# Optimization experiments

Measured on AMD Instinct MI355X. Metric: run time of the kernel, lower is better.

Reference implementation:

```python
import jax, jax.numpy as jnp
import numpy as np

CLAMP_MIN = -10.0
CLAMP_MAX = 10.0
B = 8
N = 100_000
EDGES = 3_200_000


def setup_inputs() -> dict:
    key = jax.random.key(0)
    ks = jax.random.split(key, 9)
    chem_influence = jax.random.normal(ks[0], (B, N), dtype=jnp.float32)
    E = jax.random.normal(ks[1], (B, N), dtype=jnp.float32)
    O = jax.random.normal(ks[2], (B, N), dtype=jnp.float32)
    src = jax.random.randint(ks[3], (EDGES,), 0, N, dtype=jnp.int64) if jax.config.jax_enable_x64 else jax.random.randint(ks[3], (EDGES,), 0, N).astype(jnp.int32)
    dst = jax.random.randint(ks[4], (EDGES,), 0, N).astype(src.dtype)
    w = jax.random.normal(ks[5], (EDGES,), dtype=jnp.float32)
    o_pre = jax.random.normal(ks[6], (B, N), dtype=jnp.float32)
    # learned per-neuron params (rnd_init=True ranges from the module)
    threshold = jax.random.uniform(ks[7], (N,), minval=-1.0, maxval=2.0, dtype=jnp.float32)
    decay = jax.random.uniform(ks[8], (N,), minval=0.05, maxval=1.0, dtype=jnp.float32)
    return {"chem_influence": chem_influence, "E": E, "O": O, "src": src,
            "dst": dst, "w": w, "o_pre": o_pre, "threshold": threshold, "decay": decay}


def reference(chem_influence, E, O, src, dst, w, o_pre, threshold, decay):
    # Gap-junction path: gather presyn output Oj and postsyn internal state En per edge
    Oj = o_pre[:, src]                    # (B, E)
    En = E[:, dst]                        # (B, E)
    contrib = Oj * w * jnp.sign(Oj - En)  # sign(Oj - En) * w_j * Oj
    # scatter-add edge contributions into the chemical-influence buffer (dup indices accumulate)
    chem = chem_influence.at[:, dst].add(contrib)  # (B, N)
    # Neuron dynamics (eqs 10, 11)
    S = jnp.clip(E + chem, CLAMP_MIN, CLAMP_MAX)
    gt = S > threshold
    mask = (~gt) & (S == E)
    new_o = jax.nn.relu(S - threshold)
    new_e = jnp.where(gt, new_o, jnp.where(mask, E - decay, S))
    # torch module returns (new_o, (new_e, new_o)); flatten the state tuple
    return new_o, new_e
```

## Files before the change

### kernel.cpp

```cpp
#include <hip/hip_runtime.h>

#define CLAMP_MIN_F (-10.0f)
#define CLAMP_MAX_F (10.0f)
#define BATCH 8
#define SUP_LOG 8
#define SNODES 256
#define MAXS 512
#define ESTR 9
#define EPB 16384
#define CH 2048
#define TB_BIN 1024
#define TB_ACC 1024
#define RECPT (CH / TB_ACC)
#define SPLIT 2
#define MAX4K 4096

__global__ void prep_o_kernel(const float* __restrict__ o_pre,
                              float* __restrict__ o_preT,
                              unsigned* __restrict__ total,
                              int N) {
    int n = blockIdx.x * blockDim.x + threadIdx.x;
    if (n < MAX4K) total[n] = 0u;
    if (n >= N) return;
    float o[BATCH];
    #pragma unroll
    for (int b = 0; b < BATCH; ++b) o[b] = o_pre[b * N + n];
    float4* op = (float4*)&o_preT[(size_t)n * BATCH];
    op[0] = make_float4(o[0], o[1], o[2], o[3]);
    op[1] = make_float4(o[4], o[5], o[6], o[7]);
}

__global__ __launch_bounds__(TB_BIN)
void hist_reserve_kernel(const int* __restrict__ dst,
                         unsigned* __restrict__ superTotal,
                         unsigned* __restrict__ offs0s,
                         int edges) {
    __shared__ unsigned sh[MAXS];
    int bid = blockIdx.x, tid = threadIdx.x;
    for (int s = tid; s < MAXS; s += blockDim.x) sh[s] = 0u;
    __syncthreads();
    int start = bid * EPB;
    int endE = min(edges, start + EPB);
    for (int i = start + tid; i < endE; i += blockDim.x)
        atomicAdd(&sh[((unsigned)dst[i]) >> SUP_LOG], 1u);
    __syncthreads();
    for (int s = tid; s < MAXS; s += blockDim.x) {
        unsigned c = sh[s];
        offs0s[(size_t)bid * MAXS + s] = c ? atomicAdd(&superTotal[s], c) : 0u;
    }
}

__global__ void scan4_kernel(const unsigned* __restrict__ total,
                             unsigned* __restrict__ base,
                             int KPAD) {
    __shared__ unsigned s1[1024];
    __shared__ unsigned s2[1024];
    int t = threadIdx.x;
    unsigned v0 = (4 * t     < KPAD) ? total[4 * t]     : 0u;
    unsigned v1 = (4 * t + 1 < KPAD) ? total[4 * t + 1] : 0u;
    unsigned v2 = (4 * t + 2 < KPAD) ? total[4 * t + 2] : 0u;
    unsigned v3 = (4 * t + 3 < KPAD) ? total[4 * t + 3] : 0u;
    unsigned sum = v0 + v1 + v2 + v3;
    s1[t] = sum;
    __syncthreads();
    unsigned* cur = s1;
    unsigned* nxt = s2;
    for (int off = 1; off < 1024; off <<= 1) {
        unsigned x = cur[t];
        if (t >= off) x += cur[t - off];
        __syncthreads();
        nxt[t] = x;
        __syncthreads();
        unsigned* tmp = cur; cur = nxt; nxt = tmp;
    }
    unsigned incl = cur[t];
    unsigned excl = incl - sum;
    base[4 * t]     = excl;
    base[4 * t + 1] = excl + v0;
    base[4 * t + 2] = excl + v0 + v1;
    base[4 * t + 3] = excl + v0 + v1 + v2;
    if (t == 1023) base[MAX4K] = incl;
}

__global__ __launch_bounds__(TB_BIN)
void scatter_kernel(const int* __restrict__ src,
                    const int* __restrict__ dst,
                    const float* __restrict__ w,
                    const unsigned* __restrict__ offs0s,
                    const unsigned* __restrict__ baseS,
                    int2* __restrict__ recS,
                    int edges) {
    __shared__ int2 srec[CH];
    __shared__ unsigned short ssup[CH];
    __shared__ unsigned cnt[MAXS];
    __shared__ unsigned sstart[MAXS];
    __shared__ unsigned cursor[MAXS];
    __shared__ unsigned pa[MAXS];
    __shared__ unsigned pb[MAXS];
    int bid = blockIdx.x, tid = threadIdx.x;
    for (int s = tid; s < MAXS; s += blockDim.x)
        cursor[s] = baseS[s] + offs0s[(size_t)bid * MAXS + s];
    int start = bid * EPB;
    int endE = min(edges, start + EPB);
    for (int cs = start; cs < endE; cs += CH) {
        int m = min(CH, endE - cs);
        __syncthreads();
        for (int s = tid; s < MAXS; s += blockDim.x) cnt[s] = 0u;
        __syncthreads();
        int2 hrec[2]; unsigned hsup[2], hpos[2]; bool hv[2];
        #pragma unroll
        for (int j = 0; j < 2; ++j) {
            int i = tid + j * TB_BIN;
            hv[j] = (i < m);
            if (hv[j]) {
                int gi = cs + i;
                int d = dst[gi];
                unsigned key = (((unsigned)d & (SNODES - 1)) << 17) | (unsigned)src[gi];
                hrec[j] = make_int2((int)key, __float_as_int(w[gi]));
                hsup[j] = (unsigned)d >> SUP_LOG;
                hpos[j] = atomicAdd(&cnt[hsup[j]], 1u);
            }
        }
        __syncthreads();
        {
            unsigned* cur = pa;
            unsigned* nxt = pb;
            if (tid < MAXS) cur[tid] = cnt[tid];
            __syncthreads();
            for (int off = 1; off < MAXS; off <<= 1) {
                unsigned v = 0;
                if (tid < MAXS) { v = cur[tid]; if (tid >= off) v += cur[tid - off]; }
                __syncthreads();
                if (tid < MAXS) nxt[tid] = v;
                __syncthreads();
                unsigned* t2 = cur; cur = nxt; nxt = t2;
            }
            if (tid < MAXS) sstart[tid] = cur[tid] - cnt[tid];
            __syncthreads();
        }
        #pragma unroll
        for (int j = 0; j < 2; ++j) {
            if (hv[j]) {
                unsigned idx = sstart[hsup[j]] + hpos[j];
                srec[idx] = hrec[j];
                ssup[idx] = (unsigned short)hsup[j];
            }
        }
        __syncthreads();
        #pragma unroll
        for (int j = 0; j < 2; ++j) {
            int i = tid + j * TB_BIN;
            if (i < m) {
                unsigned sup = ssup[i];
                unsigned gpos = cursor[sup] + ((unsigned)i - sstart[sup]);
                recS[gpos] = srec[i];
            }
        }
        __syncthreads();
        for (int s = tid; s < MAXS; s += blockDim.x) cursor[s] += cnt[s];
    }
}

__global__ __launch_bounds__(TB_ACC)
void accum_kernel(const int2* __restrict__ recS,
                  const unsigned* __restrict__ baseS,
                  const float* __restrict__ o_preT,
                  const float* __restrict__ E,
                  float* __restrict__ scratch,
                  int N, int BN) {
    __shared__ int2 srec[CH];
    __shared__ float e_lds[SNODES * ESTR];
    __shared__ float acc_lds[SNODES * ESTR];
    __shared__ unsigned cnt[SNODES];
    __shared__ unsigned sstart[SNODES + 1];
    int sb = blockIdx.x / SPLIT;
    int sp = blockIdx.x % SPLIT;
    int ns = sb << SUP_LOG;
    int cntn = min(SNODES, N - ns);
    int tid = threadIdx.x;

    for (int i = tid; i < SNODES * BATCH; i += TB_ACC) {
        int b = i >> SUP_LOG;
        int n = i & (SNODES - 1);
        e_lds[n * ESTR + b] = (n < cntn) ? E[(size_t)b * N + ns + n] : 0.f;
    }
    __syncthreads();

    int b = tid & 7;
    int g = tid >> 3;
    int n0 = 2 * g, n1 = 2 * g + 1;
    float En0 = e_lds[n0 * ESTR + b];
    float En1 = e_lds[n1 * ESTR + b];
    float acc0 = 0.f, acc1 = 0.f;

    unsigned r0 = baseS[sb], r1 = baseS[sb + 1];
    for (unsigned cs = r0 + (unsigned)sp * CH; cs < r1; cs += (unsigned)SPLIT * CH) {
        unsigned m = min((unsigned)CH, r1 - cs);
        if (tid < SNODES) cnt[tid] = 0u;
        __syncthreads();
        int2 hrec[RECPT]; unsigned hdl[RECPT], hpos[RECPT]; bool hv[RECPT];
        #pragma unroll
        for (int j = 0; j < RECPT; ++j) {
            unsigned i = (unsigned)tid + (unsigned)j * TB_ACC;
            hv[j] = (i < m);
            if (hv[j]) {
                int2 rec = recS[cs + i];
                unsigned dl = ((unsigned)rec.x >> 17) & (SNODES - 1);
                hrec[j] = rec;
                hdl[j] = dl;
                hpos[j] = atomicAdd(&cnt[dl], 1u);
            }
        }
        __syncthreads();
        if (tid < 64) {
            unsigned v0 = cnt[4 * tid], v1 = cnt[4 * tid + 1];
            unsigned v2 = cnt[4 * tid + 2], v3 = cnt[4 * tid + 3];
            unsigned s = v0 + v1 + v2 + v3;
            unsigned inc = s;
            #pragma unroll
            for (int off = 1; off < 64; off <<= 1) {
                unsigned t2 = __shfl_up(inc, off, 64);
                if (tid >= off) inc += t2;
            }
            unsigned excl = inc - s;
            sstart[4 * tid]     = excl;
            sstart[4 * tid + 1] = excl + v0;
            sstart[4 * tid + 2] = excl + v0 + v1;
            sstart[4 * tid + 3] = excl + v0 + v1 + v2;
            if (tid == 63) sstart[SNODES] = inc;
        }
        __syncthreads();
        #pragma unroll
        for (int j = 0; j < RECPT; ++j)
            if (hv[j]) srec[sstart[hdl[j]] + hpos[j]] = hrec[j];
        __syncthreads();
        unsigned st0 = sstart[n0];
        unsigned st1 = sstart[n1];
        unsigned en  = sstart[n1 + 1];
        for (unsigned r = st0; r < st1; ++r) {
            int2 rec = srec[r];
            unsigned si = (unsigned)rec.x & 0x1FFFFu;
            float Oj = o_preT[((size_t)si << 3) + b];
            float wv = __int_as_float(rec.y);
            float df = Oj - En0;
            float sg = (df > 0.f) ? 1.f : ((df < 0.f) ? -1.f : 0.f);
            acc0 += Oj * wv * sg;
        }
        for (unsigned r = st1; r < en; ++r) {
            int2 rec = srec[r];
            unsigned si = (unsigned)rec.x & 0x1FFFFu;
            float Oj = o_preT[((size_t)si << 3) + b];
            float wv = __int_as_float(rec.y);
            float df = Oj - En1;
            float sg = (df > 0.f) ? 1.f : ((df < 0.f) ? -1.f : 0.f);
            acc1 += Oj * wv * sg;
        }
        __syncthreads();
    }

    acc_lds[n0 * ESTR + b] = acc0;
    acc_lds[n1 * ESTR + b] = acc1;
    __syncthreads();
    float* out = &scratch[(size_t)sp * BN + (size_t)ns * BATCH];
    for (int i = tid; i < cntn * BATCH; i += TB_ACC) {
        int n = i >> 3;
        int bb = i & 7;
        out[i] = acc_lds[n * ESTR + bb];
    }
}

__global__ void finalize_g(const float* __restrict__ E,
                           const float* __restrict__ chem_in,
                           const float* __restrict__ scratch,
                           const float* __restrict__ thr,
                           const float* __restrict__ decay,
                           float* __restrict__ new_o,
                           float* __restrict__ new_e,
                           int N, int BN) {
    int n = blockIdx.x * blockDim.x + threadIdx.x;
    if (n >= N) return;
    float c[BATCH];
    #pragma unroll
    for (int b = 0; b < BATCH; ++b) c[b] = 0.f;
    #pragma unroll
    for (int g = 0; g < SPLIT; ++g) {
        const float4* cp = (const float4*)&scratch[(size_t)g * BN + (size_t)n * BATCH];
        float4 c0 = cp[0], c1 = cp[1];
        c[0]+=c0.x; c[1]+=c0.y; c[2]+=c0.z; c[3]+=c0.w;
        c[4]+=c1.x; c[5]+=c1.y; c[6]+=c1.z; c[7]+=c1.w;
    }
    float t = thr[n];
    float dc = decay[n];
    #pragma unroll
    for (int b = 0; b < BATCH; ++b) {
        int i = b * N + n;
        float e = E[i];
        float S = e + chem_in[i] + c[b];
        S = fminf(fmaxf(S, CLAMP_MIN_F), CLAMP_MAX_F);
        bool gt = S > t;
        float no = fmaxf(S - t, 0.f);
        float ne = gt ? no : ((S == e) ? (e - dc) : S);
        new_o[i] = no;
        new_e[i] = ne;
    }
}

__global__ void prep_kernel(const float* __restrict__ chem_in,
                            const float* __restrict__ o_pre,
                            const float* __restrict__ E,
                            float* __restrict__ chemT,
                            float* __restrict__ o_preT,
                            float* __restrict__ E_T,
                            int N) {
    int n = blockIdx.x * blockDim.x + threadIdx.x;
    if (n >= N) return;
    float c[BATCH], o[BATCH], ee[BATCH];
    #pragma unroll
    for (int b = 0; b < BATCH; ++b) {
        c[b]  = chem_in[b * N + n];
        o[b]  = o_pre[b * N + n];
        ee[b] = E[b * N + n];
    }
    float4* cp = (float4*)&chemT[(size_t)n * BATCH];
    cp[0] = make_float4(c[0], c[1], c[2], c[3]);
    cp[1] = make_float4(c[4], c[5], c[6], c[7]);
    float4* op = (float4*)&o_preT[(size_t)n * BATCH];
    op[0] = make_float4(o[0], o[1], o[2], o[3]);
    op[1] = make_float4(o[4], o[5], o[6], o[7]);
    float4* ep = (float4*)&E_T[(size_t)n * BATCH];
    ep[0] = make_float4(ee[0], ee[1], ee[2], ee[3]);
    ep[1] = make_float4(ee[4], ee[5], ee[6], ee[7]);
}
__global__ void edge_scatter_eb(const int* __restrict__ src,
                                const int* __restrict__ dst,
                                const float* __restrict__ w,
                                const float* __restrict__ o_preT,
                                const float* __restrict__ E_T,
                                float* __restrict__ chemT,
                                int edges) {
    int t = blockIdx.x * blockDim.x + threadIdx.x;
    int e = t >> 3;
    int b = t & 7;
    if (e >= edges) return;
    int s = src[e]; int d = dst[e]; float we = w[e];
    float Oj = o_preT[(size_t)s * BATCH + b];
    float En = E_T[(size_t)d * BATCH + b];
    float diff = Oj - En;
    float sg = (diff > 0.0f) ? 1.0f : ((diff < 0.0f) ? -1.0f : 0.0f);
    atomicAdd(&chemT[(size_t)d * BATCH + b], Oj * we * sg);
}
__global__ void finalize_nb(const float* __restrict__ E,
                            const float* __restrict__ chemT,
                            const float* __restrict__ thr,
                            const float* __restrict__ decay,
                            float* __restrict__ new_o,
                            float* __restrict__ new_e, int N) {
    int n = blockIdx.x * blockDim.x + threadIdx.x;
    if (n >= N) return;
    const float4* cp = (const float4*)&chemT[(size_t)n * BATCH];
    float4 c0 = cp[0], c1 = cp[1];
    float c[BATCH] = {c0.x, c0.y, c0.z, c0.w, c1.x, c1.y, c1.z, c1.w};
    float t = thr[n];
    float dc = decay[n];
    #pragma unroll
    for (int b = 0; b < BATCH; ++b) {
        int i = b * N + n;
        float e = E[i];
        float S = fminf(fmaxf(e + c[b], CLAMP_MIN_F), CLAMP_MAX_F);
        bool gt = S > t;
        float no = fmaxf(S - t, 0.0f);
        float ne = gt ? no : ((S == e) ? (e - dc) : S);
        new_o[i] = no;
        new_e[i] = ne;
    }
}

static inline size_t align256(size_t x) { return (x + 255) & ~(size_t)255; }

extern "C" void kernel_launch(void* const* d_in, const int* in_sizes, int n_in,
                              void* d_out, int out_size, void* d_ws, size_t ws_size,
                              hipStream_t stream) {
    const float* chem_influence = (const float*)d_in[0];
    const float* E              = (const float*)d_in[1];
    const int*   src            = (const int*)d_in[3];
    const int*   dst            = (const int*)d_in[4];
    const float* w              = (const float*)d_in[5];
    const float* o_pre          = (const float*)d_in[6];
    const float* threshold      = (const float*)d_in[7];
    const float* decay          = (const float*)d_in[8];

    const int edges = in_sizes[3];
    const int BN    = in_sizes[0];
    const int N     = in_sizes[7];

    float* new_o = (float*)d_out;
    float* new_e = (float*)d_out + BN;

    const int TB = 256;
    int nblk = (N + TB - 1) / TB;

    const int NS = (N + SNODES - 1) >> SUP_LOG;
    const int NB = (edges + EPB - 1) / EPB;

    size_t off = 0;
    size_t opreT_off  = off; off += align256((size_t)BN * 4);
    size_t base_off   = off; off += align256((size_t)(MAX4K + 1) * 4);
    size_t total_off  = off; off += align256((size_t)MAX4K * 4);
    size_t offs0_off  = off; off += align256((size_t)NB * MAXS * 4);
    size_t rec_off    = off; off += align256((size_t)edges * 8);
    size_t scr_off    = off; off += align256((size_t)SPLIT * BN * 4);
    size_t need = off;

    char* wsb = (char*)d_ws;

    if (NS <= MAXS && N <= (1 << 17) && ws_size >= need) {
        float*    o_preT  = (float*)(wsb + opreT_off);
        unsigned* baseS   = (unsigned*)(wsb + base_off);
        unsigned* total   = (unsigned*)(wsb + total_off);
        unsigned* offs0s  = (unsigned*)(wsb + offs0_off);
        int2*     recS    = (int2*)(wsb + rec_off);
        float*    scratch = (float*)(wsb + scr_off);

        prep_o_kernel<<<nblk, TB, 0, stream>>>(o_pre, o_preT, total, N);
        hist_reserve_kernel<<<NB, TB_BIN, 0, stream>>>(dst, total, offs0s, edges);
        scan4_kernel<<<1, 1024, 0, stream>>>(total, baseS, MAXS);
        scatter_kernel<<<NB, TB_BIN, 0, stream>>>(src, dst, w, offs0s, baseS,
                                                  recS, edges);
        accum_kernel<<<NS * SPLIT, TB_ACC, 0, stream>>>(recS, baseS, o_preT, E,
                                                        scratch, N, BN);
        finalize_g<<<nblk, TB, 0, stream>>>(E, chem_influence, scratch,
                                            threshold, decay, new_o, new_e, N, BN);
    } else if (ws_size >= 3 * (size_t)BN * 4) {
        float* chemT  = (float*)d_ws;
        float* o_preT = chemT + BN;
        float* E_T    = o_preT + BN;
        prep_kernel<<<nblk, TB, 0, stream>>>(chem_influence, o_pre, E,
                                             chemT, o_preT, E_T, N);
        long long ethreads = (long long)edges * BATCH;
        int gblk = (int)((ethreads + TB - 1) / TB);
        edge_scatter_eb<<<gblk, TB, 0, stream>>>(src, dst, w, o_preT, E_T,
                                                 chemT, edges);
        finalize_nb<<<nblk, TB, 0, stream>>>(E, chemT, threshold, decay,
                                             new_o, new_e, N);
    }
}
```

Before: 104.5 us.

## Split accumulation into per-chunk 256-thread blocks with variable partial count

Replaces the 1024-thread accumulation kernel (2 blocks per supernode, each looping over chunks) with 256-thread blocks, one per 2048-record chunk, up to 8 per supernode. Blocks with no chunk exit early. Each thread now owns 8 nodes for one batch lane instead of 2, and finalize sums a variable number of partial buffers taken from the supernode record counts. The aim is finer-grained scheduling and more blocks in flight. In exchange, each thread runs longer serial gather loops, and more partial sums are written to and read from scratch.

```diff
diff --git a/kernel.cpp b/kernel.cpp
--- a/kernel.cpp
+++ b/kernel.cpp
@@ -6,21 +6,19 @@
 #define SUP_LOG 8
 #define SNODES 256
 #define MAXS 512
-#define ESTR 9
+#define ASTR 9
 #define EPB 16384
 #define CH 2048
+#define MAXCH 8
 #define TB_BIN 1024
-#define TB_ACC 1024
-#define RECPT (CH / TB_ACC)
-#define SPLIT 2
 #define MAX4K 4096
 
 __global__ void prep_o_kernel(const float* __restrict__ o_pre,
                               float* __restrict__ o_preT,
-                              unsigned* __restrict__ total,
+                              unsigned* __restrict__ superTotal,
                               int N) {
     int n = blockIdx.x * blockDim.x + threadIdx.x;
-    if (n < MAX4K) total[n] = 0u;
+    if (n < MAXS) superTotal[n] = 0u;
     if (n >= N) return;
     float o[BATCH];
     #pragma unroll
@@ -161,54 +159,58 @@
     }
 }
 
-__global__ __launch_bounds__(TB_ACC)
-void accum_kernel(const int2* __restrict__ recS,
-                  const unsigned* __restrict__ baseS,
-                  const float* __restrict__ o_preT,
-                  const float* __restrict__ E,
-                  float* __restrict__ scratch,
-                  int N, int BN) {
+__global__ __launch_bounds__(256)
+void accum_chunk_kernel(const int2* __restrict__ recS,
+                        const unsigned* __restrict__ baseS,
+                        const float* __restrict__ o_preT,
+                        const float* __restrict__ E,
+                        float* __restrict__ scratch,
+                        int N, int BN) {
     __shared__ int2 srec[CH];
-    __shared__ float e_lds[SNODES * ESTR];
-    __shared__ float acc_lds[SNODES * ESTR];
+    __shared__ float e_lds[SNODES * ASTR];
+    __shared__ float acc_st[SNODES * ASTR];
     __shared__ unsigned cnt[SNODES];
     __shared__ unsigned sstart[SNODES + 1];
-    int sb = blockIdx.x / SPLIT;
-    int sp = blockIdx.x % SPLIT;
+    int sb = blockIdx.x / MAXCH;
+    int sp = blockIdx.x % MAXCH;
+    unsigned r0 = baseS[sb], r1 = baseS[sb + 1];
+    unsigned nrec = r1 - r0;
+    if (nrec == 0) return;
+    unsigned nch = (nrec + CH - 1) / CH;
+    if ((unsigned)sp >= nch) return;
     int ns = sb << SUP_LOG;
-    int cntn = min(SNODES, N - ns);
+    int cnt_n = min(SNODES, N - ns);
     int tid = threadIdx.x;
 
-    for (int i = tid; i < SNODES * BATCH; i += TB_ACC) {
+    for (int i = tid; i < SNODES * BATCH; i += 256) {
         int b = i >> SUP_LOG;
         int n = i & (SNODES - 1);
-        e_lds[n * ESTR + b] = (n < cntn) ? E[(size_t)b * N + ns + n] : 0.f;
+        if (n < cnt_n) e_lds[n * ASTR + b] = E[(size_t)b * N + ns + n];
     }
     __syncthreads();
 
     int b = tid & 7;
     int g = tid >> 3;
-    int n0 = 2 * g, n1 = 2 * g + 1;
-    float En0 = e_lds[n0 * ESTR + b];
-    float En1 = e_lds[n1 * ESTR + b];
-    float acc0 = 0.f, acc1 = 0.f;
-
-    unsigned r0 = baseS[sb], r1 = baseS[sb + 1];
-    for (unsigned cs = r0 + (unsigned)sp * CH; cs < r1; cs += (unsigned)SPLIT * CH) {
+    float acc[8];
+    #pragma unroll
+    for (int j = 0; j < 8; ++j) acc[j] = 0.f;
+
+    for (unsigned cs = r0 + (unsigned)sp * CH; cs < r1; cs += (unsigned)MAXCH * CH) {
         unsigned m = min((unsigned)CH, r1 - cs);
-        if (tid < SNODES) cnt[tid] = 0u;
-        __syncthreads();
-        int2 hrec[RECPT]; unsigned hdl[RECPT], hpos[RECPT]; bool hv[RECPT];
-        #pragma unroll
-        for (int j = 0; j < RECPT; ++j) {
-            unsigned i = (unsigned)tid + (unsigned)j * TB_ACC;
-            hv[j] = (i < m);
-            if (hv[j]) {
+        cnt[tid] = 0u;
+        __syncthreads();
+        int2 hrec[8]; unsigned hmeta[8];
+        #pragma unroll
+        for (int j = 0; j < 8; ++j) {
+            unsigned i = (unsigned)tid + (unsigned)j * 256u;
+            if (i < m) {
                 int2 rec = recS[cs + i];
                 unsigned dl = ((unsigned)rec.x >> 17) & (SNODES - 1);
+                unsigned pos = atomicAdd(&cnt[dl], 1u);
                 hrec[j] = rec;
-                hdl[j] = dl;
-                hpos[j] = atomicAdd(&cnt[dl], 1u);
+                hmeta[j] = (dl << 16) | pos;
+            } else {
+                hmeta[j] = 0xFFFFFFFFu;
             }
         }
         __syncthreads();
@@ -231,47 +233,50 @@
         }
         __syncthreads();
         #pragma unroll
-        for (int j = 0; j < RECPT; ++j)
-            if (hv[j]) srec[sstart[hdl[j]] + hpos[j]] = hrec[j];
-        __syncthreads();
-        unsigned st0 = sstart[n0];
-        unsigned st1 = sstart[n1];
-        unsigned en  = sstart[n1 + 1];
-        for (unsigned r = st0; r < st1; ++r) {
-            int2 rec = srec[r];
-            unsigned si = (unsigned)rec.x & 0x1FFFFu;
-            float Oj = o_preT[((size_t)si << 3) + b];
-            float wv = __int_as_float(rec.y);
-            float df = Oj - En0;
-            float sg = (df > 0.f) ? 1.f : ((df < 0.f) ? -1.f : 0.f);
-            acc0 += Oj * wv * sg;
-        }
-        for (unsigned r = st1; r < en; ++r) {
-            int2 rec = srec[r];
-            unsigned si = (unsigned)rec.x & 0x1FFFFu;
-            float Oj = o_preT[((size_t)si << 3) + b];
-            float wv = __int_as_float(rec.y);
-            float df = Oj - En1;
-            float sg = (df > 0.f) ? 1.f : ((df < 0.f) ? -1.f : 0.f);
-            acc1 += Oj * wv * sg;
-        }
-        __syncthreads();
-    }
-
-    acc_lds[n0 * ESTR + b] = acc0;
-    acc_lds[n1 * ESTR + b] = acc1;
+        for (int j = 0; j < 8; ++j) {
+            if (hmeta[j] != 0xFFFFFFFFu) {
+                unsigned dl = hmeta[j] >> 16;
+                unsigned pos = hmeta[j] & 0xFFFFu;
+                srec[sstart[dl] + pos] = hrec[j];
+            }
+        }
+        __syncthreads();
+        #pragma unroll
+        for (int j = 0; j < 8; ++j) {
+            int node = 32 * j + g;
+            float En = e_lds[node * ASTR + b];
+            unsigned st = sstart[node];
+            unsigned en = st + cnt[node];
+            float a = acc[j];
+            for (unsigned r = st; r < en; ++r) {
+                int2 rec = srec[r];
+                unsigned si = (unsigned)rec.x & 0x1FFFFu;
+                float Oj = o_preT[((size_t)si << 3) + b];
+                float wv = __int_as_float(rec.y);
+                float df = Oj - En;
+                float sg = (df > 0.f) ? 1.f : ((df < 0.f) ? -1.f : 0.f);
+                a += Oj * wv * sg;
+            }
+            acc[j] = a;
+        }
+        __syncthreads();
+    }
+
+    #pragma unroll
+    for (int j = 0; j < 8; ++j) acc_st[(32 * j + g) * ASTR + b] = acc[j];
     __syncthreads();
     float* out = &scratch[(size_t)sp * BN + (size_t)ns * BATCH];
-    for (int i = tid; i < cntn * BATCH; i += TB_ACC) {
+    for (int i = tid; i < cnt_n * BATCH; i += 256) {
         int n = i >> 3;
         int bb = i & 7;
-        out[i] = acc_lds[n * ESTR + bb];
+        out[i] = acc_st[n * ASTR + bb];
     }
 }
 
 __global__ void finalize_g(const float* __restrict__ E,
                            const float* __restrict__ chem_in,
                            const float* __restrict__ scratch,
+                           const unsigned* __restrict__ baseS,
                            const float* __restrict__ thr,
                            const float* __restrict__ decay,
                            float* __restrict__ new_o,
@@ -279,11 +284,14 @@
                            int N, int BN) {
     int n = blockIdx.x * blockDim.x + threadIdx.x;
     if (n >= N) return;
+    int s = n >> SUP_LOG;
+    unsigned nrec = baseS[s + 1] - baseS[s];
+    int nch = (int)((nrec + CH - 1) / CH);
+    if (nch > MAXCH) nch = MAXCH;
     float c[BATCH];
     #pragma unroll
     for (int b = 0; b < BATCH; ++b) c[b] = 0.f;
-    #pragma unroll
-    for (int g = 0; g < SPLIT; ++g) {
+    for (int g = 0; g < nch; ++g) {
         const float4* cp = (const float4*)&scratch[(size_t)g * BN + (size_t)n * BATCH];
         float4 c0 = cp[0], c1 = cp[1];
         c[0]+=c0.x; c[1]+=c0.y; c[2]+=c0.z; c[3]+=c0.w;
@@ -405,10 +413,10 @@
     size_t off = 0;
     size_t opreT_off  = off; off += align256((size_t)BN * 4);
     size_t base_off   = off; off += align256((size_t)(MAX4K + 1) * 4);
-    size_t total_off  = off; off += align256((size_t)MAX4K * 4);
+    size_t total_off  = off; off += align256((size_t)MAXS * 4);
     size_t offs0_off  = off; off += align256((size_t)NB * MAXS * 4);
     size_t rec_off    = off; off += align256((size_t)edges * 8);
-    size_t scr_off    = off; off += align256((size_t)SPLIT * BN * 4);
+    size_t scr_off    = off; off += align256((size_t)MAXCH * BN * 4);
     size_t need = off;
 
     char* wsb = (char*)d_ws;
@@ -416,19 +424,19 @@
     if (NS <= MAXS && N <= (1 << 17) && ws_size >= need) {
         float*    o_preT  = (float*)(wsb + opreT_off);
         unsigned* baseS   = (unsigned*)(wsb + base_off);
-        unsigned* total   = (unsigned*)(wsb + total_off);
+        unsigned* supTot  = (unsigned*)(wsb + total_off);
         unsigned* offs0s  = (unsigned*)(wsb + offs0_off);
         int2*     recS    = (int2*)(wsb + rec_off);
         float*    scratch = (float*)(wsb + scr_off);
 
-        prep_o_kernel<<<nblk, TB, 0, stream>>>(o_pre, o_preT, total, N);
-        hist_reserve_kernel<<<NB, TB_BIN, 0, stream>>>(dst, total, offs0s, edges);
-        scan4_kernel<<<1, 1024, 0, stream>>>(total, baseS, MAXS);
+        prep_o_kernel<<<nblk, TB, 0, stream>>>(o_pre, o_preT, supTot, N);
+        hist_reserve_kernel<<<NB, TB_BIN, 0, stream>>>(dst, supTot, offs0s, edges);
+        scan4_kernel<<<1, 1024, 0, stream>>>(supTot, baseS, MAXS);
         scatter_kernel<<<NB, TB_BIN, 0, stream>>>(src, dst, w, offs0s, baseS,
                                                   recS, edges);
-        accum_kernel<<<NS * SPLIT, TB_ACC, 0, stream>>>(recS, baseS, o_preT, E,
-                                                        scratch, N, BN);
-        finalize_g<<<nblk, TB, 0, stream>>>(E, chem_influence, scratch,
+        accum_chunk_kernel<<<NS * MAXCH, 256, 0, stream>>>(recS, baseS, o_preT,
+                                                           E, scratch, N, BN);
+        finalize_g<<<nblk, TB, 0, stream>>>(E, chem_influence, scratch, baseS,
                                             threshold, decay, new_o, new_e, N, BN);
     } else if (ws_size >= 3 * (size_t)BN * 4) {
         float* chemT  = (float*)d_ws;
```

After: 156.7 us. 49.9% more time.
